# Optimization experiments

Hardware: AMD Instinct MI355X
Metric: run time of the kernel (lower is better)

Reference implementation:

```python
import jax, jax.numpy as jnp
import numpy as np

B, S, D, H, K, F, L, V = 2, 2048, 512, 8, 64, 2048, 4, 32000  # batch, seq, d_model, heads, head_dim, ff, layers, vocab


def setup_inputs() -> dict:
    key = jax.random.key(0)
    ks = jax.random.split(key, 10)
    s = 0.02
    HK = H * K
    return {
        "x": jax.random.randint(ks[0], (B, S), 0, V, dtype=jnp.int64),
        "emb": jax.random.normal(ks[1], (V, D), jnp.float32) * s,
        "pos": jax.random.normal(ks[2], (S, D), jnp.float32) * s,
        "Wq": jax.random.normal(ks[3], (L, D, HK), jnp.float32) * s,
        "bq": jnp.zeros((L, HK), jnp.float32),
        "Wk": jax.random.normal(ks[4], (L, D, HK), jnp.float32) * s,
        "bk": jnp.zeros((L, HK), jnp.float32),
        "Wv": jax.random.normal(ks[5], (L, D, HK), jnp.float32) * s,
        "bv": jnp.zeros((L, HK), jnp.float32),
        "Wo": jax.random.normal(ks[6], (L, HK, D), jnp.float32) * s,
        "bo": jnp.zeros((L, D), jnp.float32),
        "W1": jax.random.normal(ks[7], (L, D, F), jnp.float32) * s,
        "b1": jnp.zeros((L, F), jnp.float32),
        "W2": jax.random.normal(ks[8], (L, F, D), jnp.float32) * s,
        "b2": jnp.zeros((L, D), jnp.float32),
    }


def _forward(x, emb, pos, Wq, bq, Wk, bk, Wv, bv, Wo, bo, W1, b1, W2, b2):
    b, s = x.shape
    h = emb[x] + pos[:s][None]  # [B,S,D]
    causal = jnp.triu(jnp.ones((s, s), dtype=bool), 1)  # True above diagonal -> masked
    scale = 1.0 / jnp.sqrt(jnp.float32(K))

    def layer(h, p):
        wq, bq_, wk, bk_, wv, bv_, wo, bo_, w1, b1_, w2, b2_ = p
        q = (h @ wq + bq_).reshape(b, s, H, K).transpose(0, 2, 1, 3)  # [B,H,S,K]
        k = (h @ wk + bk_).reshape(b, s, H, K).transpose(0, 2, 1, 3)
        v = (h @ wv + bv_).reshape(b, s, H, K).transpose(0, 2, 1, 3)
        scores = jnp.einsum("bhqk,bhsk->bhqs", q, k) * scale  # [B,H,S,S]
        scores = jnp.where(causal, -jnp.inf, scores)
        attn = jax.nn.softmax(scores, axis=-1)
        o = jnp.einsum("bhqs,bhsk->bhqk", attn, v)  # [B,H,S,K]
        o = o.transpose(0, 2, 1, 3).reshape(b, s, H * K)
        h = h + (o @ wo + bo_)
        ff = jax.nn.relu(h @ w1 + b1_) @ w2 + b2_
        return h + ff, None

    h, _ = jax.lax.scan(layer, h, (Wq, bq, Wk, bk, Wv, bv, Wo, bo, W1, b1, W2, b2))
    return h


def reference(x, emb, pos, Wq, bq, Wk, bk, Wv, bv, Wo, bo, W1, b1, W2, b2):
    return _forward(x, emb, pos, Wq, bq, Wk, bk, Wv, bv, Wo, bo, W1, b1, W2, b2)
```

## Files before the change

### kernel.cpp

```cpp
#include <hip/hip_runtime.h>

typedef __bf16 bf16x8 __attribute__((ext_vector_type(8)));
typedef float f32x4 __attribute__((ext_vector_type(4)));
typedef float f32x16 __attribute__((ext_vector_type(16)));
typedef unsigned short u16;
typedef unsigned int u32;

static constexpr int B = 2, S = 2048, D = 512, H = 8, HD = 64, F = 2048, L = 4, HK = 512, M = 4096;

__device__ __forceinline__ u16 f2bf(float f) {
  u32 u = __float_as_uint(f);
  u = (u + 0x7fffu + ((u >> 16) & 1u)) >> 16;
  return (u16)u;
}

__device__ __forceinline__ u32 pk2(float lo, float hi) {
  return (u32)f2bf(lo) | ((u32)f2bf(hi) << 16);
}

__device__ __forceinline__ f32x4 mfma16(bf16x8 a, bf16x8 b, f32x4 c) {
  return __builtin_amdgcn_mfma_f32_16x16x32_bf16(a, b, c, 0, 0, 0);
}

__device__ __forceinline__ f32x16 mfma32(bf16x8 a, bf16x8 b, f32x16 c) {
  return __builtin_amdgcn_mfma_f32_32x32x16_bf16(a, b, c, 0, 0, 0);
}

__device__ __forceinline__ void gload_lds16(const u16* g, u16* l) {
  __builtin_amdgcn_global_load_lds((const __attribute__((address_space(1))) void*)g,
                                   (__attribute__((address_space(3))) void*)l, 16, 0, 0);
}

__global__ __launch_bounds__(256) void wtrans_kernel(const float* __restrict__ in,
                                                     u16* __restrict__ out,
                                                     int R, int C, int ostride) {
  __shared__ float tile[32][33];
  in += (size_t)blockIdx.z * R * C;
  out += (size_t)blockIdx.z * ostride;
  int r0 = blockIdx.x * 32, c0 = blockIdx.y * 32;
  int tx = threadIdx.x, ty = threadIdx.y;
  #pragma unroll
  for (int i = ty; i < 32; i += 8)
    tile[i][tx] = in[(size_t)(r0 + i) * C + c0 + tx];
  __syncthreads();
  #pragma unroll
  for (int i = ty; i < 32; i += 8)
    out[(size_t)(c0 + i) * R + r0 + tx] = f2bf(tile[tx][i]);
}

__global__ __launch_bounds__(256) void embed_kernel(const int* __restrict__ x,
                                                    const float* __restrict__ emb,
                                                    const float* __restrict__ pos,
                                                    float* __restrict__ hf,
                                                    u16* __restrict__ hb) {
  int idx = blockIdx.x * 256 + threadIdx.x;
  int dc = idx & 127;
  int bs = idx >> 7;
  int s = bs & (S - 1);
  int tok = x[bs];
  float4 e = ((const float4*)(emb + (size_t)tok * D))[dc];
  float4 p = ((const float4*)(pos + (size_t)s * D))[dc];
  float4 v;
  v.x = e.x + p.x; v.y = e.y + p.y; v.z = e.z + p.z; v.w = e.w + p.w;
  ((float4*)hf)[idx] = v;
  ushort4 u;
  u.x = f2bf(v.x); u.y = f2bf(v.y); u.z = f2bf(v.z); u.w = f2bf(v.w);
  ((ushort4*)hb)[idx] = u;
}

template <int BM, int KD>
__device__ __forceinline__ void gemm_core(const u16* __restrict__ A,
                                          const u16* __restrict__ Wt,
                                          u16* lds, f32x4 (&acc)[4][4]) {
  constexpr int WN = (BM == 128) ? 2 : 4;
  constexpr int NI = 8 / WN;
  constexpr int MI = 4;
  const int t = threadIdx.x;
  const int lane = t & 63, w = t >> 6;
  const int lr = lane & 15, lg = lane >> 4;
  const int wm = w / WN, wn = w % WN;
  const int r0 = blockIdx.x * BM, c0 = blockIdx.y * 128;
  u16* ldsA = lds;
  u16* ldsB = lds + BM * 32;
  const int srow = t >> 2, scol = (t & 3) * 8;
  const u16* gA = A + (size_t)(r0 + srow) * KD + scol;
  const u16* gB = Wt + (size_t)(c0 + srow) * KD + scol;
  const int ldsw = w * 512;

  for (int k0 = 0; k0 < KD; k0 += 32) {
    gload_lds16(gA + k0, ldsA + ldsw);
    if (BM == 128) gload_lds16(gA + (size_t)64 * KD + k0, ldsA + 2048 + ldsw);
    gload_lds16(gB + k0, ldsB + ldsw);
    gload_lds16(gB + (size_t)64 * KD + k0, ldsB + 2048 + ldsw);
    __syncthreads();
    bf16x8 a[MI], b[NI];
    #pragma unroll
    for (int i = 0; i < MI; i++)
      a[i] = *(const bf16x8*)(ldsA + (wm * 64 + i * 16 + lr) * 32 + lg * 8);
    #pragma unroll
    for (int j = 0; j < NI; j++)
      b[j] = *(const bf16x8*)(ldsB + (wn * NI * 16 + j * 16 + lr) * 32 + lg * 8);
    #pragma unroll
    for (int i = 0; i < MI; i++)
      #pragma unroll
      for (int j = 0; j < NI; j++)
        acc[i][j] = mfma16(a[i], b[j], acc[i][j]);
    __syncthreads();
  }
}

__global__ __launch_bounds__(256) void gemm_qkv_kernel(const u16* __restrict__ A,
                                                       const u16* __restrict__ Wt,
                                                       const float* __restrict__ bq,
                                                       const float* __restrict__ bk,
                                                       const float* __restrict__ bv,
                                                       u16* __restrict__ q,
                                                       u16* __restrict__ k,
                                                       u16* __restrict__ v) {
  __shared__ u16 lds[8192];
  f32x4 acc[4][4] = {};
  gemm_core<128, 512>(A, Wt, lds, acc);
  const int lane = threadIdx.x & 63, w = threadIdx.x >> 6;
  const int lr = lane & 15, lg = lane >> 4;
  const int wm = w >> 1, wn = w & 1;
  const int r0 = blockIdx.x * 128, c0 = blockIdx.y * 128;
  #pragma unroll
  for (int j = 0; j < 4; j++) {
    int col = c0 + wn * 64 + j * 16 + lr;
    int sel = col >> 9, cc = col & 511;
    u16* outp = (sel == 0) ? q : (sel == 1) ? k : v;
    const float* bp = (sel == 0) ? bq : (sel == 1) ? bk : bv;
    float bias = bp[cc];
    #pragma unroll
    for (int i = 0; i < 4; i++) {
      int rbase = r0 + wm * 64 + i * 16 + lg * 4;
      #pragma unroll
      for (int r = 0; r < 4; r++)
        outp[(size_t)(rbase + r) * 512 + cc] = f2bf(acc[i][j][r] + bias);
    }
  }
}

__global__ __launch_bounds__(256) void gemm_ff1_kernel(const u16* __restrict__ A,
                                                       const u16* __restrict__ Wt,
                                                       const float* __restrict__ bias,
                                                       u16* __restrict__ out) {
  __shared__ u16 lds[8192];
  f32x4 acc[4][4] = {};
  gemm_core<128, 512>(A, Wt, lds, acc);
  const int lane = threadIdx.x & 63, w = threadIdx.x >> 6;
  const int lr = lane & 15, lg = lane >> 4;
  const int wm = w >> 1, wn = w & 1;
  const int r0 = blockIdx.x * 128, c0 = blockIdx.y * 128;
  #pragma unroll
  for (int j = 0; j < 4; j++) {
    int col = c0 + wn * 64 + j * 16 + lr;
    float bv = bias[col];
    #pragma unroll
    for (int i = 0; i < 4; i++) {
      int rbase = r0 + wm * 64 + i * 16 + lg * 4;
      #pragma unroll
      for (int r = 0; r < 4; r++)
        out[(size_t)(rbase + r) * F + col] = f2bf(fmaxf(acc[i][j][r] + bv, 0.f));
    }
  }
}

template <int KD>
__global__ __launch_bounds__(256) void gemm_resid_kernel(const u16* __restrict__ A,
                                                         const u16* __restrict__ Wt,
                                                         const float* __restrict__ bias,
                                                         float* __restrict__ hf,
                                                         u16* __restrict__ hb) {
  __shared__ u16 lds[6144];
  f32x4 acc[4][4] = {};
  gemm_core<64, KD>(A, Wt, lds, acc);
  const int lane = threadIdx.x & 63, w = threadIdx.x >> 6;
  const int lr = lane & 15, lg = lane >> 4;
  const int wn = w;
  const int r0 = blockIdx.x * 64, c0 = blockIdx.y * 128;
  #pragma unroll
  for (int j = 0; j < 2; j++) {
    int col = c0 + wn * 32 + j * 16 + lr;
    float bv = bias[col];
    #pragma unroll
    for (int i = 0; i < 4; i++) {
      int rbase = r0 + i * 16 + lg * 4;
      #pragma unroll
      for (int r = 0; r < 4; r++) {
        size_t idx = (size_t)(rbase + r) * D + col;
        float v = hf[idx] + acc[i][j][r] + bv;
        hf[idx] = v;
        hb[idx] = f2bf(v);
      }
    }
  }
}

__global__ __launch_bounds__(256) void vtrans_kernel(const u16* __restrict__ v,
                                                     u16* __restrict__ vt) {
  __shared__ u16 tile[64][65];
  int bh = blockIdx.x, b = bh >> 3, h = bh & 7;
  int s0 = blockIdx.y * 64;
  int t = threadIdx.x;
  union V16 { uint4 v4[2]; u16 e[16]; };
  {
    int sl = t >> 2, cc = (t & 3) * 16;
    const u16* src = v + (size_t)(b * S + s0 + sl) * HK + h * 64 + cc;
    V16 tv;
    tv.v4[0] = *(const uint4*)src;
    tv.v4[1] = *(const uint4*)(src + 8);
    #pragma unroll
    for (int i = 0; i < 16; i++) tile[sl][cc + i] = tv.e[i];
  }
  __syncthreads();
  {
    int kd = t >> 2, sc = (t & 3) * 16;
    V16 tv;
    #pragma unroll
    for (int i = 0; i < 16; i++) tv.e[i] = tile[sc + i][kd];
    u16* dst = vt + ((size_t)bh * 64 + kd) * S + s0 + sc;
    *(uint4*)dst = tv.v4[0];
    *(uint4*)(dst + 8) = tv.v4[1];
  }
}

__device__ __forceinline__ void load_kv(const u16* kbase, const u16* vbase,
                                        int kv0, int ql, int hi,
                                        bf16x8 (&kf)[4], bf16x8 (&vf)[4]) {
  const u16* kr = kbase + (size_t)(kv0 + ql) * HK;
  #pragma unroll
  for (int kc = 0; kc < 4; kc++) kf[kc] = *(const bf16x8*)(kr + kc * 16 + hi * 8);
  #pragma unroll
  for (int km = 0; km < 2; km++)
    #pragma unroll
    for (int dt = 0; dt < 2; dt++)
      vf[km * 2 + dt] = *(const bf16x8*)(vbase + (size_t)(dt * 32 + ql) * S + kv0 + km * 16 + hi * 8);
}

__global__ __launch_bounds__(256) void attn32_kernel(const u16* __restrict__ q,
                                                     const u16* __restrict__ k,
                                                     const u16* __restrict__ vt,
                                                     u16* __restrict__ o) {
  __shared__ float lds_o[4][64][32];
  __shared__ float lds_m[4][32];
  __shared__ float lds_l[4][32];
  int bh = blockIdx.x, b = bh >> 3, h = bh & 7;
  int w = threadIdx.x >> 6, lane = threadIdx.x & 63;
  int tile = 63 - blockIdx.y;
  int q0 = tile * 32;
  int ql = lane & 31, hi = lane >> 5;
  int qa = q0 + ql;

  const u16* qrow = q + (size_t)(b * S + qa) * HK + h * 64;
  bf16x8 qf[4];
  #pragma unroll
  for (int kc = 0; kc < 4; kc++) qf[kc] = *(const bf16x8*)(qrow + kc * 16 + hi * 8);

  const u16* kbase = k + (size_t)(b * S) * HK + h * 64;
  const u16* vbase = vt + (size_t)bh * 64 * S;

  f32x16 oacc[2] = {};
  float mrun = -3.0e38f, lrun = 0.f;
  int cnt = (w <= tile) ? ((tile - w) >> 2) + 1 : 0;
  int s = w;

  bf16x8 kf[4], vf[4], kn[4], vn[4];
  if (cnt > 0) load_kv(kbase, vbase, s * 32, ql, hi, kf, vf);

  for (int i = 0; i < cnt; i++) {
    if (i + 1 < cnt) load_kv(kbase, vbase, (s + 4) * 32, ql, hi, kn, vn);
    int kv0 = s * 32;
    f32x16 sacc = {};
    #pragma unroll
    for (int kc = 0; kc < 4; kc++) sacc = mfma32(kf[kc], qf[kc], sacc);

    float p[16];
    if (s == tile) {
      #pragma unroll
      for (int r = 0; r < 16; r++) {
        int kva = kv0 + (r & 3) + 8 * (r >> 2) + 4 * hi;
        p[r] = (kva > qa) ? -1e30f : sacc[r] * 0.125f;
      }
    } else {
      #pragma unroll
      for (int r = 0; r < 16; r++) p[r] = sacc[r] * 0.125f;
    }

    float mx = fmaxf(fmaxf(fmaxf(p[0], p[1]), fmaxf(p[2], p[3])),
                     fmaxf(fmaxf(p[4], p[5]), fmaxf(p[6], p[7])));
    float mx2 = fmaxf(fmaxf(fmaxf(p[8], p[9]), fmaxf(p[10], p[11])),
                      fmaxf(fmaxf(p[12], p[13]), fmaxf(p[14], p[15])));
    mx = fmaxf(mx, mx2);
    mx = fmaxf(mx, __shfl_xor(mx, 32));
    float mnew = fmaxf(mrun, mx);
    float corr = __expf(mrun - mnew);
    mrun = mnew;
    #pragma unroll
    for (int r = 0; r < 16; r++) p[r] = __expf(p[r] - mnew);
    float ps = ((p[0] + p[1]) + (p[2] + p[3])) + ((p[4] + p[5]) + (p[6] + p[7]))
             + ((p[8] + p[9]) + (p[10] + p[11])) + ((p[12] + p[13]) + (p[14] + p[15]));
    ps += __shfl_xor(ps, 32);
    lrun = lrun * corr + ps;
    #pragma unroll
    for (int dt = 0; dt < 2; dt++)
      #pragma unroll
      for (int r = 0; r < 16; r++) oacc[dt][r] *= corr;

    #pragma unroll
    for (int km = 0; km < 2; km++) {
      int base = 8 * km;
      u32 a0_01 = pk2(p[base + 0], p[base + 1]);
      u32 a0_23 = pk2(p[base + 2], p[base + 3]);
      u32 a1_01 = pk2(p[base + 4], p[base + 5]);
      u32 a1_23 = pk2(p[base + 6], p[base + 7]);
      u32 send1 = hi ? a0_01 : a1_01;
      u32 send2 = hi ? a0_23 : a1_23;
      u32 recv1 = __shfl_xor(send1, 32);
      u32 recv2 = __shfl_xor(send2, 32);
      union { u32 wd[4]; bf16x8 v; } pf;
      if (hi == 0) { pf.wd[0] = a0_01; pf.wd[1] = a0_23; pf.wd[2] = recv1; pf.wd[3] = recv2; }
      else         { pf.wd[0] = recv1; pf.wd[1] = recv2; pf.wd[2] = a1_01; pf.wd[3] = a1_23; }
      oacc[0] = mfma32(vf[km * 2 + 0], pf.v, oacc[0]);
      oacc[1] = mfma32(vf[km * 2 + 1], pf.v, oacc[1]);
    }
    #pragma unroll
    for (int j = 0; j < 4; j++) { kf[j] = kn[j]; vf[j] = vn[j]; }
    s += 4;
  }

  if (hi == 0) { lds_m[w][ql] = mrun; lds_l[w][ql] = lrun; }
  #pragma unroll
  for (int dt = 0; dt < 2; dt++)
    #pragma unroll
    for (int r = 0; r < 16; r++) {
      int d = dt * 32 + (r & 3) + 8 * (r >> 2) + 4 * hi;
      lds_o[w][d][ql] = oacc[dt][r];
    }
  __syncthreads();

  float m0 = lds_m[0][ql], m1 = lds_m[1][ql], m2 = lds_m[2][ql], m3 = lds_m[3][ql];
  float Mx = fmaxf(fmaxf(m0, m1), fmaxf(m2, m3));
  float s0 = __expf(m0 - Mx), s1 = __expf(m1 - Mx), s2 = __expf(m2 - Mx), s3 = __expf(m3 - Mx);
  float Ls = lds_l[0][ql] * s0 + lds_l[1][ql] * s1 + lds_l[2][ql] * s2 + lds_l[3][ql] * s3;
  float inv = 1.0f / Ls;
  int dbase = w * 16 + hi * 8;
  union { uint4 u4; u16 e[8]; } outv;
  #pragma unroll
  for (int j = 0; j < 8; j++) {
    int d = dbase + j;
    float v = (lds_o[0][d][ql] * s0 + lds_o[1][d][ql] * s1 +
               lds_o[2][d][ql] * s2 + lds_o[3][d][ql] * s3) * inv;
    outv.e[j] = f2bf(v);
  }
  *(uint4*)(o + (size_t)(b * S + qa) * HK + h * 64 + dbase) = outv.u4;
}

extern "C" void kernel_launch(void* const* d_in, const int* in_sizes, int n_in,
                              void* d_out, int out_size, void* d_ws, size_t ws_size,
                              hipStream_t stream) {
  const int* x = (const int*)d_in[0];
  const float* emb = (const float*)d_in[1];
  const float* pos = (const float*)d_in[2];
  const float* Wq = (const float*)d_in[3];
  const float* bq = (const float*)d_in[4];
  const float* Wk = (const float*)d_in[5];
  const float* bk = (const float*)d_in[6];
  const float* Wv = (const float*)d_in[7];
  const float* bv = (const float*)d_in[8];
  const float* Wo = (const float*)d_in[9];
  const float* bo = (const float*)d_in[10];
  const float* W1 = (const float*)d_in[11];
  const float* b1 = (const float*)d_in[12];
  const float* W2 = (const float*)d_in[13];
  const float* b2 = (const float*)d_in[14];
  float* hf = (float*)d_out;

  char* p = (char*)d_ws;
  const size_t SZ_MD = (size_t)M * D * 2;
  u16* h_bf = (u16*)p;  p += SZ_MD;
  u16* q_bf = (u16*)p;  p += SZ_MD;
  u16* k_bf = (u16*)p;  p += SZ_MD;
  u16* v_bf = (u16*)p;  p += SZ_MD;
  u16* vt_bf = (u16*)p; p += SZ_MD;
  u16* o_bf = (u16*)p;  p += SZ_MD;
  u16* ff_bf = (u16*)p; p += (size_t)M * F * 2;
  u16* WqkvT = (u16*)p; p += (size_t)L * D * (3 * HK) * 2;
  u16* WoT = (u16*)p;   p += (size_t)L * HK * D * 2;
  u16* W1T = (u16*)p;   p += (size_t)L * D * F * 2;
  u16* W2T = (u16*)p;   p += (size_t)L * F * D * 2;

  dim3 tb(32, 8);
  const int QKV_L = 3 * HK * D;
  wtrans_kernel<<<dim3(D / 32, HK / 32, L), tb, 0, stream>>>(Wq, WqkvT, D, HK, QKV_L);
  wtrans_kernel<<<dim3(D / 32, HK / 32, L), tb, 0, stream>>>(Wk, WqkvT + HK * D, D, HK, QKV_L);
  wtrans_kernel<<<dim3(D / 32, HK / 32, L), tb, 0, stream>>>(Wv, WqkvT + 2 * HK * D, D, HK, QKV_L);
  wtrans_kernel<<<dim3(HK / 32, D / 32, L), tb, 0, stream>>>(Wo, WoT, HK, D, HK * D);
  wtrans_kernel<<<dim3(D / 32, F / 32, L), tb, 0, stream>>>(W1, W1T, D, F, D * F);
  wtrans_kernel<<<dim3(F / 32, D / 32, L), tb, 0, stream>>>(W2, W2T, F, D, F * D);

  embed_kernel<<<(M * D / 4) / 256, 256, 0, stream>>>(x, emb, pos, hf, h_bf);

  for (int l = 0; l < L; ++l) {
    gemm_qkv_kernel<<<dim3(M / 128, (3 * HK) / 128), 256, 0, stream>>>(
        h_bf, WqkvT + (size_t)l * QKV_L, bq + l * HK, bk + l * HK, bv + l * HK,
        q_bf, k_bf, v_bf);
    vtrans_kernel<<<dim3(B * H, S / 64), 256, 0, stream>>>(v_bf, vt_bf);
    attn32_kernel<<<dim3(B * H, 64), 256, 0, stream>>>(q_bf, k_bf, vt_bf, o_bf);
    gemm_resid_kernel<512><<<dim3(M / 64, D / 128), 256, 0, stream>>>(
        o_bf, WoT + (size_t)l * HK * D, bo + l * D, hf, h_bf);
    gemm_ff1_kernel<<<dim3(M / 128, F / 128), 256, 0, stream>>>(
        h_bf, W1T + (size_t)l * D * F, b1 + l * F, ff_bf);
    gemm_resid_kernel<2048><<<dim3(M / 64, D / 128), 256, 0, stream>>>(
        ff_bf, W2T + (size_t)l * F * D, b2 + l * D, hf, h_bf);
  }
}
```

Measured before the change: 691.0 us.

## Widen GEMM K-tile with swizzled LDS and streamline attention softmax

The GEMM core now stages 64-wide K slices per iteration instead of 32, with an XOR swizzle on LDS columns to avoid bank conflicts, halving the barrier count and doubling shared memory per block. The attention kernel folds the scale into an exp2 with a premultiplied constant, skips the running-max rescale unless any lane's max exceeds a threshold (lazy rescaling), defers the cross-half sum reduction to the end, and packs bf16 by truncation via a byte permute instead of round-to-nearest. Risks include lower occupancy from larger LDS, and slightly different numerics from truncating the probabilities and from lazy rescaling.

```diff
diff --git a/kernel.cpp b/kernel.cpp
--- a/kernel.cpp
+++ b/kernel.cpp
@@ -14,8 +14,8 @@
   return (u16)u;
 }
 
-__device__ __forceinline__ u32 pk2(float lo, float hi) {
-  return (u32)f2bf(lo) | ((u32)f2bf(hi) << 16);
+__device__ __forceinline__ u32 pk2t(float lo, float hi2) {
+  return __builtin_amdgcn_perm(__float_as_uint(hi2), __float_as_uint(lo), 0x07060302u);
 }
 
 __device__ __forceinline__ f32x4 mfma16(bf16x8 a, bf16x8 b, f32x4 c) {
@@ -74,37 +74,47 @@
                                           u16* lds, f32x4 (&acc)[4][4]) {
   constexpr int WN = (BM == 128) ? 2 : 4;
   constexpr int NI = 8 / WN;
-  constexpr int MI = 4;
   const int t = threadIdx.x;
   const int lane = t & 63, w = t >> 6;
   const int lr = lane & 15, lg = lane >> 4;
   const int wm = w / WN, wn = w % WN;
   const int r0 = blockIdx.x * BM, c0 = blockIdx.y * 128;
   u16* ldsA = lds;
-  u16* ldsB = lds + BM * 32;
-  const int srow = t >> 2, scol = (t & 3) * 8;
+  u16* ldsB = lds + BM * 64;
+  const int srow = t >> 3;
+  const int scol = (((t & 7) ^ (srow & 7)) * 8);
   const u16* gA = A + (size_t)(r0 + srow) * KD + scol;
   const u16* gB = Wt + (size_t)(c0 + srow) * KD + scol;
-  const int ldsw = w * 512;
-
-  for (int k0 = 0; k0 < KD; k0 += 32) {
-    gload_lds16(gA + k0, ldsA + ldsw);
-    if (BM == 128) gload_lds16(gA + (size_t)64 * KD + k0, ldsA + 2048 + ldsw);
-    gload_lds16(gB + k0, ldsB + ldsw);
-    gload_lds16(gB + (size_t)64 * KD + k0, ldsB + 2048 + ldsw);
+  const int ldst = t * 8;
+  const int gsw = lr & 7;
+
+  for (int k0 = 0; k0 < KD; k0 += 64) {
+    #pragma unroll
+    for (int r = 0; r < BM / 32; r++)
+      gload_lds16(gA + (size_t)(r * 32) * KD + k0, ldsA + r * 2048 + ldst);
+    #pragma unroll
+    for (int r = 0; r < 4; r++)
+      gload_lds16(gB + (size_t)(r * 32) * KD + k0, ldsB + r * 2048 + ldst);
     __syncthreads();
-    bf16x8 a[MI], b[NI];
-    #pragma unroll
-    for (int i = 0; i < MI; i++)
-      a[i] = *(const bf16x8*)(ldsA + (wm * 64 + i * 16 + lr) * 32 + lg * 8);
-    #pragma unroll
-    for (int j = 0; j < NI; j++)
-      b[j] = *(const bf16x8*)(ldsB + (wn * NI * 16 + j * 16 + lr) * 32 + lg * 8);
-    #pragma unroll
-    for (int i = 0; i < MI; i++)
-      #pragma unroll
-      for (int j = 0; j < NI; j++)
-        acc[i][j] = mfma16(a[i], b[j], acc[i][j]);
+    #pragma unroll
+    for (int kk = 0; kk < 2; kk++) {
+      bf16x8 a[4], b[NI];
+      #pragma unroll
+      for (int i = 0; i < 4; i++) {
+        int row = wm * 64 + i * 16 + lr;
+        a[i] = *(const bf16x8*)(ldsA + row * 64 + (((kk * 4 + lg) ^ gsw) * 8));
+      }
+      #pragma unroll
+      for (int j = 0; j < NI; j++) {
+        int row = wn * NI * 16 + j * 16 + lr;
+        b[j] = *(const bf16x8*)(ldsB + row * 64 + (((kk * 4 + lg) ^ gsw) * 8));
+      }
+      #pragma unroll
+      for (int i = 0; i < 4; i++)
+        #pragma unroll
+        for (int j = 0; j < NI; j++)
+          acc[i][j] = mfma16(a[i], b[j], acc[i][j]);
+    }
     __syncthreads();
   }
 }
@@ -117,7 +127,7 @@
                                                        u16* __restrict__ q,
                                                        u16* __restrict__ k,
                                                        u16* __restrict__ v) {
-  __shared__ u16 lds[8192];
+  __shared__ u16 lds[16384];
   f32x4 acc[4][4] = {};
   gemm_core<128, 512>(A, Wt, lds, acc);
   const int lane = threadIdx.x & 63, w = threadIdx.x >> 6;
@@ -145,7 +155,7 @@
                                                        const u16* __restrict__ Wt,
                                                        const float* __restrict__ bias,
                                                        u16* __restrict__ out) {
-  __shared__ u16 lds[8192];
+  __shared__ u16 lds[16384];
   f32x4 acc[4][4] = {};
   gemm_core<128, 512>(A, Wt, lds, acc);
   const int lane = threadIdx.x & 63, w = threadIdx.x >> 6;
@@ -172,7 +182,7 @@
                                                          const float* __restrict__ bias,
                                                          float* __restrict__ hf,
                                                          u16* __restrict__ hb) {
-  __shared__ u16 lds[6144];
+  __shared__ u16 lds[12288];
   f32x4 acc[4][4] = {};
   gemm_core<64, KD>(A, Wt, lds, acc);
   const int lane = threadIdx.x & 63, w = threadIdx.x >> 6;
@@ -247,10 +257,12 @@
   __shared__ float lds_l[4][32];
   int bh = blockIdx.x, b = bh >> 3, h = bh & 7;
   int w = threadIdx.x >> 6, lane = threadIdx.x & 63;
-  int tile = 63 - blockIdx.y;
+  int tile = 63 - (int)blockIdx.y;
   int q0 = tile * 32;
   int ql = lane & 31, hi = lane >> 5;
   int qa = q0 + ql;
+  constexpr float c2 = 0.18033688f;
+  constexpr float THR = 44.3614f;
 
   const u16* qrow = q + (size_t)(b * S + qa) * HK + h * 64;
   bf16x8 qf[4];
@@ -261,7 +273,10 @@
   const u16* vbase = vt + (size_t)bh * 64 * S;
 
   f32x16 oacc[2] = {};
-  float mrun = -3.0e38f, lrun = 0.f;
+  float mraw = -3.0e38f;
+  float m2 = mraw * c2;
+  float thr = mraw;
+  float lsum = 0.f;
   int cnt = (w <= tile) ? ((tile - w) >> 2) + 1 : 0;
   int s = w;
 
@@ -275,45 +290,45 @@
     #pragma unroll
     for (int kc = 0; kc < 4; kc++) sacc = mfma32(kf[kc], qf[kc], sacc);
 
-    float p[16];
     if (s == tile) {
       #pragma unroll
       for (int r = 0; r < 16; r++) {
         int kva = kv0 + (r & 3) + 8 * (r >> 2) + 4 * hi;
-        p[r] = (kva > qa) ? -1e30f : sacc[r] * 0.125f;
+        if (kva > qa) sacc[r] = -3.0e38f;
       }
-    } else {
-      #pragma unroll
-      for (int r = 0; r < 16; r++) p[r] = sacc[r] * 0.125f;
-    }
-
-    float mx = fmaxf(fmaxf(fmaxf(p[0], p[1]), fmaxf(p[2], p[3])),
-                     fmaxf(fmaxf(p[4], p[5]), fmaxf(p[6], p[7])));
-    float mx2 = fmaxf(fmaxf(fmaxf(p[8], p[9]), fmaxf(p[10], p[11])),
-                      fmaxf(fmaxf(p[12], p[13]), fmaxf(p[14], p[15])));
-    mx = fmaxf(mx, mx2);
+    }
+
+    float mx = fmaxf(fmaxf(fmaxf(fmaxf(sacc[0], sacc[1]), fmaxf(sacc[2], sacc[3])),
+                           fmaxf(fmaxf(sacc[4], sacc[5]), fmaxf(sacc[6], sacc[7]))),
+                     fmaxf(fmaxf(fmaxf(sacc[8], sacc[9]), fmaxf(sacc[10], sacc[11])),
+                           fmaxf(fmaxf(sacc[12], sacc[13]), fmaxf(sacc[14], sacc[15]))));
     mx = fmaxf(mx, __shfl_xor(mx, 32));
-    float mnew = fmaxf(mrun, mx);
-    float corr = __expf(mrun - mnew);
-    mrun = mnew;
-    #pragma unroll
-    for (int r = 0; r < 16; r++) p[r] = __expf(p[r] - mnew);
-    float ps = ((p[0] + p[1]) + (p[2] + p[3])) + ((p[4] + p[5]) + (p[6] + p[7]))
-             + ((p[8] + p[9]) + (p[10] + p[11])) + ((p[12] + p[13]) + (p[14] + p[15]));
-    ps += __shfl_xor(ps, 32);
-    lrun = lrun * corr + ps;
-    #pragma unroll
-    for (int dt = 0; dt < 2; dt++)
-      #pragma unroll
-      for (int r = 0; r < 16; r++) oacc[dt][r] *= corr;
+    if (__any(mx > thr)) {
+      float mnew = fmaxf(mraw, mx);
+      float corr = exp2f((mraw - mnew) * c2);
+      mraw = mnew;
+      m2 = mraw * c2;
+      thr = mraw + THR;
+      lsum *= corr;
+      #pragma unroll
+      for (int dt = 0; dt < 2; dt++)
+        #pragma unroll
+        for (int r = 0; r < 16; r++) oacc[dt][r] *= corr;
+    }
+
+    float p[16];
+    #pragma unroll
+    for (int r = 0; r < 16; r++) p[r] = exp2f(fmaf(sacc[r], c2, -m2));
+    lsum += (((p[0] + p[1]) + (p[2] + p[3])) + ((p[4] + p[5]) + (p[6] + p[7])))
+          + (((p[8] + p[9]) + (p[10] + p[11])) + ((p[12] + p[13]) + (p[14] + p[15])));
 
     #pragma unroll
     for (int km = 0; km < 2; km++) {
       int base = 8 * km;
-      u32 a0_01 = pk2(p[base + 0], p[base + 1]);
-      u32 a0_23 = pk2(p[base + 2], p[base + 3]);
-      u32 a1_01 = pk2(p[base + 4], p[base + 5]);
-      u32 a1_23 = pk2(p[base + 6], p[base + 7]);
+      u32 a0_01 = pk2t(p[base + 0], p[base + 1]);
+      u32 a0_23 = pk2t(p[base + 2], p[base + 3]);
+      u32 a1_01 = pk2t(p[base + 4], p[base + 5]);
+      u32 a1_23 = pk2t(p[base + 6], p[base + 7]);
       u32 send1 = hi ? a0_01 : a1_01;
       u32 send2 = hi ? a0_23 : a1_23;
       u32 recv1 = __shfl_xor(send1, 32);
@@ -328,8 +343,9 @@
     for (int j = 0; j < 4; j++) { kf[j] = kn[j]; vf[j] = vn[j]; }
     s += 4;
   }
-
-  if (hi == 0) { lds_m[w][ql] = mrun; lds_l[w][ql] = lrun; }
+  float lrun = lsum + __shfl_xor(lsum, 32);
+
+  if (hi == 0) { lds_m[w][ql] = mraw; lds_l[w][ql] = lrun; }
   #pragma unroll
   for (int dt = 0; dt < 2; dt++)
     #pragma unroll
@@ -339,9 +355,10 @@
     }
   __syncthreads();
 
-  float m0 = lds_m[0][ql], m1 = lds_m[1][ql], m2 = lds_m[2][ql], m3 = lds_m[3][ql];
-  float Mx = fmaxf(fmaxf(m0, m1), fmaxf(m2, m3));
-  float s0 = __expf(m0 - Mx), s1 = __expf(m1 - Mx), s2 = __expf(m2 - Mx), s3 = __expf(m3 - Mx);
+  float m0 = lds_m[0][ql], m1 = lds_m[1][ql], m2c = lds_m[2][ql], m3 = lds_m[3][ql];
+  float Mx = fmaxf(fmaxf(m0, m1), fmaxf(m2c, m3));
+  float s0 = exp2f((m0 - Mx) * c2), s1 = exp2f((m1 - Mx) * c2);
+  float s2 = exp2f((m2c - Mx) * c2), s3 = exp2f((m3 - Mx) * c2);
   float Ls = lds_l[0][ql] * s0 + lds_l[1][ql] * s1 + lds_l[2][ql] * s2 + lds_l[3][ql] * s3;
   float inv = 1.0f / Ls;
   int dbase = w * 16 + hi * 8;
```

Measured after the change: 654.9 us. 5.2% less time.
